# Performance work log

Measured on AMD Instinct MI355X. Metric: run time of the kernel, lower is better.

Reference implementation:

```python
import jax, jax.numpy as jnp
import numpy as np

B, S, I, H = 128, 512, 256, 512


def _lstm_last_hidden(x, W_ih, W_hh, b_ih, b_hh):
    """Single-layer unidirectional LSTM (PyTorch gate order i,f,g,o).
    x: [B,S,I]; returns final hidden state h_n [B,H]."""
    Hd = W_hh.shape[1]
    # Precompute input-side gate activations for all timesteps: [S,B,4H]
    xg = jnp.einsum('bsi,gi->sbg', x, W_ih) + b_ih + b_hh

    def step(carry, gx):
        h, c = carry
        g = gx + h @ W_hh.T  # [B,4H]
        i, f, gg, o = jnp.split(g, 4, axis=-1)
        i = jax.nn.sigmoid(i)
        f = jax.nn.sigmoid(f)
        gg = jnp.tanh(gg)
        o = jax.nn.sigmoid(o)
        c = f * c + i * gg
        h = o * jnp.tanh(c)
        return (h, c), None

    h0 = jnp.zeros((x.shape[0], Hd), x.dtype)
    (h_n, _), _ = jax.lax.scan(step, (h0, h0), xg)
    return h_n


def setup_inputs() -> dict:
    key = jax.random.key(0)
    k1, k2, k3, k4, k5, k6 = jax.random.split(key, 6)
    s = 1.0 / np.sqrt(H)  # PyTorch LSTM init scale
    return {
        'text_one': jax.random.normal(k1, (B, S, I), jnp.float32),
        'text_two': jax.random.normal(k2, (B, S, I), jnp.float32),
        'W_ih': jax.random.normal(k3, (4 * H, I), jnp.float32) * s,
        'W_hh': jax.random.normal(k4, (4 * H, H), jnp.float32) * s,
        'b_ih': jax.random.normal(k5, (4 * H,), jnp.float32) * s,
        'b_hh': jax.random.normal(k6, (4 * H,), jnp.float32) * s,
    }


def reference(text_one, text_two, W_ih, W_hh, b_ih, b_hh):
    out1 = _lstm_last_hidden(text_one, W_ih, W_hh, b_ih, b_hh)
    out2 = _lstm_last_hidden(text_two, W_ih, W_hh, b_ih, b_hh)
    return (out1, out2)
```

## Files before the change

### kernel.cpp

```cpp
#include <hip/hip_runtime.h>
#include <stdint.h>

#define SLEN    512
#define IDIM    256
#define HDIM    512
#define NROW    256
#define KP      776
#define NSTEP   512
#define NGRP    16
#define GWG     16

typedef __attribute__((ext_vector_type(8))) _Float16 half8;
typedef __attribute__((ext_vector_type(4))) float   f32x4;
typedef __attribute__((ext_vector_type(4))) int     i32x4;

#define AS1 __attribute__((address_space(1)))
#define AS3 __attribute__((address_space(3)))

__device__ __forceinline__ float sigm(float x)   { return 1.0f / (1.0f + __expf(-x)); }
__device__ __forceinline__ float tanh_f(float x) { return 2.0f / (1.0f + __expf(-2.0f * x)) - 1.0f; }

__device__ __forceinline__ half8 cvt8(float4 a, float4 b) {
    half8 v;
    v[0] = (_Float16)a.x; v[1] = (_Float16)a.y; v[2] = (_Float16)a.z; v[3] = (_Float16)a.w;
    v[4] = (_Float16)b.x; v[5] = (_Float16)b.y; v[6] = (_Float16)b.z; v[7] = (_Float16)b.w;
    return v;
}
__device__ __forceinline__ half8 cvt8i(i32x4 a, i32x4 b) {
    float4 fa = *(float4*)&a, fb = *(float4*)&b;
    return cvt8(fa, fb);
}

union hu { _Float16 h; unsigned short u; };

__global__ __launch_bounds__(256, 1)
void lstm_persistent(const float* __restrict__ x0, const float* __restrict__ x1,
                     const float* __restrict__ wih, const float* __restrict__ whh,
                     const float* __restrict__ bih, const float* __restrict__ bhh,
                     _Float16* __restrict__ hb, int* __restrict__ flg,
                     float* __restrict__ out) {
    __shared__ __align__(16) _Float16 Ab[16 * KP];

    const int tid  = threadIdx.x;
    const int lane = tid & 63;
    const int w    = tid >> 6;
    const int quad = lane >> 4;
    const int l16  = lane & 15;
    const int igrp = blockIdx.x & 15;
    const int jcg  = blockIdx.x >> 4;

    const int q0  = l16 & 3, ccl = l16 >> 2;
    const int colb = jcg * 32 + w * 8 + ccl * 2;
    const int gc0 = q0 * HDIM + colb;
    const int gc1 = gc0 + 1;
    half8 wf0[24], wf1[24];
#pragma unroll
    for (int kk = 0; kk < 24; ++kk) {
        int k0 = kk * 32 + quad * 8;
        const float* sA = (k0 < IDIM) ? wih + (size_t)gc0 * IDIM + k0
                                      : whh + (size_t)gc0 * HDIM + (k0 - IDIM);
        const float* sB = (k0 < IDIM) ? wih + (size_t)gc1 * IDIM + k0
                                      : whh + (size_t)gc1 * HDIM + (k0 - IDIM);
        wf0[kk] = cvt8(*(const float4*)sA, *(const float4*)(sA + 4));
        wf1[kk] = cvt8(*(const float4*)sB, *(const float4*)(sB + 4));
    }

    float bias0[4], bias1[4];
#pragma unroll
    for (int q = 0; q < 4; ++q) {
        int g0 = q * HDIM + jcg * 32 + w * 8 + quad * 2;
        bias0[q] = bih[g0] + bhh[g0];
        bias1[q] = bih[g0 + 1] + bhh[g0 + 1];
    }

    const float* xp  = (igrp < 8) ? x0 : x1;
    const int   brow = (igrp & 7) * 16;
    const int   r0   = tid >> 5;
    const int   o0   = (tid & 31) * 8;
    const int   grow = igrp * 16 + l16;
    const int   cc0  = jcg * 32 + w * 8 + quad * 2;

    const int* fpoll = flg + igrp * 64 + lane;
    int*       fmine = flg + igrp * 64 + jcg * 4 + w;

    float c0 = 0.f, c1 = 0.f;
    int gaveup = 0;

    {
        const float* xr0 = xp + ((size_t)(brow + r0) * SLEN + 0) * IDIM + o0;
        const float* xr1 = xr0 + (size_t)8 * SLEN * IDIM;
        float4 pa = *(const float4*)xr0, pb = *(const float4*)(xr0 + 4);
        float4 pc = *(const float4*)xr1, pd = *(const float4*)(xr1 + 4);
        *(half8*)&Ab[r0 * KP + o0]       = cvt8(pa, pb);
        *(half8*)&Ab[(r0 + 8) * KP + o0] = cvt8(pc, pd);
    }
    __syncthreads();

#pragma unroll 1
    for (int t = 0; t < NSTEP; ++t) {
        if (t > 0) {
            asm volatile("s_waitcnt lgkmcnt(0)" ::: "memory");
            __builtin_amdgcn_sched_barrier(0);
            __builtin_amdgcn_s_barrier();
        }

        f32x4 acc0 = {bias0[0], bias0[1], bias0[2], bias0[3]};
        f32x4 acc1 = {bias1[0], bias1[1], bias1[2], bias1[3]};
        const _Float16* ab = &Ab[l16 * KP + quad * 8];
#pragma unroll
        for (int kk = 0; kk < 8; ++kk) {
            half8 bf = *(const half8*)(ab + kk * 32);
            acc0 = __builtin_amdgcn_mfma_f32_16x16x32_f16(wf0[kk], bf, acc0, 0, 0, 0);
            acc1 = __builtin_amdgcn_mfma_f32_16x16x32_f16(wf1[kk], bf, acc1, 0, 0, 0);
        }

        if (t > 0 && !gaveup) {
            int it = 0;
            while (true) {
                int f;
                asm volatile("global_load_dword %0, %1, off sc0 sc1\n\t"
                             "s_waitcnt vmcnt(0)"
                             : "=&v"(f) : "v"(fpoll) : "memory");
                if (__all(f >= t)) break;
                __builtin_amdgcn_s_sleep(1);
                if (++it > (1 << 20)) { gaveup = 1; break; }
            }
            __builtin_amdgcn_fence(__ATOMIC_ACQUIRE, "workgroup");
        }

        {
            const _Float16* hsrc = hb + (size_t)((t + 1) & 1) * (NROW * HDIM)
                                      + (size_t)(igrp * 16) * HDIM;
#pragma unroll
            for (int p = 0; p < 4; ++p) {
                const int r = p * 4 + w;
                const _Float16* g = hsrc + (size_t)r * HDIM + lane * 8;
                __builtin_amdgcn_global_load_lds(
                    (const AS1 void*)g, (AS3 void*)&Ab[r * KP + IDIM],
                    16, 0, 17);
            }
            asm volatile("s_waitcnt vmcnt(0)" ::: "memory");
            __builtin_amdgcn_sched_barrier(0);
        }

        i32x4 xv0, xv1, xv2, xv3;
        if (t < NSTEP - 1) {
            const float* xr0 = xp + ((size_t)(brow + r0) * SLEN + (t + 1)) * IDIM + o0;
            const float* xr1 = xr0 + (size_t)8 * SLEN * IDIM;
            asm volatile(
                "global_load_dwordx4 %0, %4, off\n\t"
                "global_load_dwordx4 %1, %4, off offset:16\n\t"
                "global_load_dwordx4 %2, %5, off\n\t"
                "global_load_dwordx4 %3, %5, off offset:16"
                : "=&v"(xv0), "=&v"(xv1), "=&v"(xv2), "=&v"(xv3)
                : "v"(xr0), "v"(xr1)
                : "memory");
        }
        __builtin_amdgcn_sched_barrier(0);
        __builtin_amdgcn_s_barrier();

#pragma unroll
        for (int kk = 8; kk < 24; ++kk) {
            half8 bf = *(const half8*)(ab + kk * 32);
            acc0 = __builtin_amdgcn_mfma_f32_16x16x32_f16(wf0[kk], bf, acc0, 0, 0, 0);
            acc1 = __builtin_amdgcn_mfma_f32_16x16x32_f16(wf1[kk], bf, acc1, 0, 0, 0);
        }

        float i0 = sigm(acc0[0]), f0 = sigm(acc0[1]), g0 = tanh_f(acc0[2]), o0g = sigm(acc0[3]);
        c0 = f0 * c0 + i0 * g0;
        float h0 = o0g * tanh_f(c0);
        float i1 = sigm(acc1[0]), f1 = sigm(acc1[1]), g1 = tanh_f(acc1[2]), o1g = sigm(acc1[3]);
        c1 = f1 * c1 + i1 * g1;
        float h1 = o1g * tanh_f(c1);

        if (t < NSTEP - 1) {
            _Float16* hd = hb + (size_t)(t & 1) * (NROW * HDIM) + (size_t)grow * HDIM;
            hu u0; u0.h = (_Float16)h0;
            hu u1; u1.h = (_Float16)h1;
            unsigned int hp = (unsigned int)u0.u | ((unsigned int)u1.u << 16);
            asm volatile("global_store_dword %0, %1, off sc0 sc1"
                         :: "v"((int*)(hd + cc0)), "v"(hp) : "memory");
            __builtin_amdgcn_sched_barrier(0);
            asm volatile("s_waitcnt vmcnt(0)" ::: "memory");
            __builtin_amdgcn_sched_barrier(0);
            if (lane == 0) {
                int fv = t + 1;
                asm volatile("global_store_dword %0, %1, off sc0 sc1"
                             :: "v"(fmine), "v"(fv) : "memory");
            }
            *(half8*)&Ab[r0 * KP + o0]       = cvt8i(xv0, xv1);
            *(half8*)&Ab[(r0 + 8) * KP + o0] = cvt8i(xv2, xv3);
        } else {
            float2 ov; ov.x = h0; ov.y = h1;
            *(float2*)(out + (size_t)grow * HDIM + cc0) = ov;
        }
    }
}

extern "C" void kernel_launch(void* const* d_in, const int* in_sizes, int n_in,
                              void* d_out, int out_size, void* d_ws, size_t ws_size,
                              hipStream_t stream) {
    const float* x0  = (const float*)d_in[0];
    const float* x1  = (const float*)d_in[1];
    const float* wih = (const float*)d_in[2];
    const float* whh = (const float*)d_in[3];
    const float* bih = (const float*)d_in[4];
    const float* bhh = (const float*)d_in[5];

    _Float16* hb = (_Float16*)d_ws;
    int* flg = (int*)((char*)d_ws + (size_t)2 * NROW * HDIM * sizeof(_Float16));
    size_t zbytes = (size_t)2 * NROW * HDIM * sizeof(_Float16)
                  + (size_t)NGRP * 64 * sizeof(int);
    hipMemsetAsync(d_ws, 0, zbytes, stream);

    lstm_persistent<<<dim3(256), dim3(256), 0, stream>>>(
        x0, x1, wih, whh, bih, bhh, hb, flg, (float*)d_out);
}
```

Measured before the change: 1.563 ms.

## Keep x operand in registers and prefetch flag poll to skip LDS barrier

Each lane now loads its own slice of the next timestep's input directly into registers and feeds it to the MFMA B operand, so x no longer passes through LDS. This removes the top-of-loop lgkmcnt wait and workgroup barrier. It also issues a speculative flag load right after publishing h, so the spin loop can be skipped when the neighbours have already finished. The cost is 16 redundant, less coalesced global loads per lane per step (each 16-lane column group re-reads x), plus extra VGPR pressure on top of the 48 weight fragments.

```diff
diff --git a/kernel.cpp b/kernel.cpp
--- a/kernel.cpp
+++ b/kernel.cpp
@@ -5,7 +5,7 @@
 #define IDIM    256
 #define HDIM    512
 #define NROW    256
-#define KP      776
+#define HPH     520
 #define NSTEP   512
 #define NGRP    16
 #define GWG     16
@@ -26,10 +26,6 @@
     v[4] = (_Float16)b.x; v[5] = (_Float16)b.y; v[6] = (_Float16)b.z; v[7] = (_Float16)b.w;
     return v;
 }
-__device__ __forceinline__ half8 cvt8i(i32x4 a, i32x4 b) {
-    float4 fa = *(float4*)&a, fb = *(float4*)&b;
-    return cvt8(fa, fb);
-}
 
 union hu { _Float16 h; unsigned short u; };
 
@@ -39,7 +35,7 @@
                      const float* __restrict__ bih, const float* __restrict__ bhh,
                      _Float16* __restrict__ hb, int* __restrict__ flg,
                      float* __restrict__ out) {
-    __shared__ __align__(16) _Float16 Ab[16 * KP];
+    __shared__ __align__(16) _Float16 Abh[16 * HPH];
 
     const int tid  = threadIdx.x;
     const int lane = tid & 63;
@@ -75,55 +71,50 @@
 
     const float* xp  = (igrp < 8) ? x0 : x1;
     const int   brow = (igrp & 7) * 16;
-    const int   r0   = tid >> 5;
-    const int   o0   = (tid & 31) * 8;
     const int   grow = igrp * 16 + l16;
     const int   cc0  = jcg * 32 + w * 8 + quad * 2;
 
+    const float* xrow = xp + (size_t)(brow + l16) * SLEN * IDIM + quad * 8;
+
     const int* fpoll = flg + igrp * 64 + lane;
     int*       fmine = flg + igrp * 64 + jcg * 4 + w;
 
     float c0 = 0.f, c1 = 0.f;
     int gaveup = 0;
-
-    {
-        const float* xr0 = xp + ((size_t)(brow + r0) * SLEN + 0) * IDIM + o0;
-        const float* xr1 = xr0 + (size_t)8 * SLEN * IDIM;
-        float4 pa = *(const float4*)xr0, pb = *(const float4*)(xr0 + 4);
-        float4 pc = *(const float4*)xr1, pd = *(const float4*)(xr1 + 4);
-        *(half8*)&Ab[r0 * KP + o0]       = cvt8(pa, pb);
-        *(half8*)&Ab[(r0 + 8) * KP + o0] = cvt8(pc, pd);
-    }
-    __syncthreads();
+    int pf = 0;
+
+    half8 xf[8];
+#pragma unroll
+    for (int kk = 0; kk < 8; ++kk) {
+        const float* p = xrow + (size_t)kk * 32;
+        xf[kk] = cvt8(*(const float4*)p, *(const float4*)(p + 4));
+    }
 
 #pragma unroll 1
     for (int t = 0; t < NSTEP; ++t) {
-        if (t > 0) {
-            asm volatile("s_waitcnt lgkmcnt(0)" ::: "memory");
-            __builtin_amdgcn_sched_barrier(0);
-            __builtin_amdgcn_s_barrier();
-        }
-
         f32x4 acc0 = {bias0[0], bias0[1], bias0[2], bias0[3]};
         f32x4 acc1 = {bias1[0], bias1[1], bias1[2], bias1[3]};
-        const _Float16* ab = &Ab[l16 * KP + quad * 8];
 #pragma unroll
         for (int kk = 0; kk < 8; ++kk) {
-            half8 bf = *(const half8*)(ab + kk * 32);
-            acc0 = __builtin_amdgcn_mfma_f32_16x16x32_f16(wf0[kk], bf, acc0, 0, 0, 0);
-            acc1 = __builtin_amdgcn_mfma_f32_16x16x32_f16(wf1[kk], bf, acc1, 0, 0, 0);
-        }
+            acc0 = __builtin_amdgcn_mfma_f32_16x16x32_f16(wf0[kk], xf[kk], acc0, 0, 0, 0);
+            acc1 = __builtin_amdgcn_mfma_f32_16x16x32_f16(wf1[kk], xf[kk], acc1, 0, 0, 0);
+        }
+        __builtin_amdgcn_sched_barrier(0);
 
         if (t > 0 && !gaveup) {
-            int it = 0;
-            while (true) {
-                int f;
-                asm volatile("global_load_dword %0, %1, off sc0 sc1\n\t"
-                             "s_waitcnt vmcnt(0)"
-                             : "=&v"(f) : "v"(fpoll) : "memory");
-                if (__all(f >= t)) break;
-                __builtin_amdgcn_s_sleep(1);
-                if (++it > (1 << 20)) { gaveup = 1; break; }
+            asm volatile("s_waitcnt vmcnt(0)" ::: "memory");
+            __builtin_amdgcn_sched_barrier(0);
+            if (!__all(pf >= t)) {
+                int it = 0;
+                while (true) {
+                    int f;
+                    asm volatile("global_load_dword %0, %1, off sc0 sc1\n\t"
+                                 "s_waitcnt vmcnt(0)"
+                                 : "=&v"(f) : "v"(fpoll) : "memory");
+                    if (__all(f >= t)) break;
+                    __builtin_amdgcn_s_sleep(1);
+                    if (++it > (1 << 20)) { gaveup = 1; break; }
+                }
             }
             __builtin_amdgcn_fence(__ATOMIC_ACQUIRE, "workgroup");
         }
@@ -136,34 +127,51 @@
                 const int r = p * 4 + w;
                 const _Float16* g = hsrc + (size_t)r * HDIM + lane * 8;
                 __builtin_amdgcn_global_load_lds(
-                    (const AS1 void*)g, (AS3 void*)&Ab[r * KP + IDIM],
+                    (const AS1 void*)g, (AS3 void*)&Abh[r * HPH],
                     16, 0, 17);
             }
             asm volatile("s_waitcnt vmcnt(0)" ::: "memory");
             __builtin_amdgcn_sched_barrier(0);
         }
 
-        i32x4 xv0, xv1, xv2, xv3;
+        i32x4 xr0_, xr1_, xr2_, xr3_, xr4_, xr5_, xr6_, xr7_;
+        i32x4 xr8_, xr9_, xrA_, xrB_, xrC_, xrD_, xrE_, xrF_;
         if (t < NSTEP - 1) {
-            const float* xr0 = xp + ((size_t)(brow + r0) * SLEN + (t + 1)) * IDIM + o0;
-            const float* xr1 = xr0 + (size_t)8 * SLEN * IDIM;
+            const float* xb = xrow + (size_t)(t + 1) * IDIM;
             asm volatile(
-                "global_load_dwordx4 %0, %4, off\n\t"
-                "global_load_dwordx4 %1, %4, off offset:16\n\t"
-                "global_load_dwordx4 %2, %5, off\n\t"
-                "global_load_dwordx4 %3, %5, off offset:16"
-                : "=&v"(xv0), "=&v"(xv1), "=&v"(xv2), "=&v"(xv3)
-                : "v"(xr0), "v"(xr1)
-                : "memory");
+                "global_load_dwordx4 %0, %8, off\n\t"
+                "global_load_dwordx4 %1, %8, off offset:16\n\t"
+                "global_load_dwordx4 %2, %8, off offset:128\n\t"
+                "global_load_dwordx4 %3, %8, off offset:144\n\t"
+                "global_load_dwordx4 %4, %8, off offset:256\n\t"
+                "global_load_dwordx4 %5, %8, off offset:272\n\t"
+                "global_load_dwordx4 %6, %8, off offset:384\n\t"
+                "global_load_dwordx4 %7, %8, off offset:400"
+                : "=&v"(xr0_), "=&v"(xr1_), "=&v"(xr2_), "=&v"(xr3_),
+                  "=&v"(xr4_), "=&v"(xr5_), "=&v"(xr6_), "=&v"(xr7_)
+                : "v"(xb) : "memory");
+            asm volatile(
+                "global_load_dwordx4 %0, %8, off offset:512\n\t"
+                "global_load_dwordx4 %1, %8, off offset:528\n\t"
+                "global_load_dwordx4 %2, %8, off offset:640\n\t"
+                "global_load_dwordx4 %3, %8, off offset:656\n\t"
+                "global_load_dwordx4 %4, %8, off offset:768\n\t"
+                "global_load_dwordx4 %5, %8, off offset:784\n\t"
+                "global_load_dwordx4 %6, %8, off offset:896\n\t"
+                "global_load_dwordx4 %7, %8, off offset:912"
+                : "=&v"(xr8_), "=&v"(xr9_), "=&v"(xrA_), "=&v"(xrB_),
+                  "=&v"(xrC_), "=&v"(xrD_), "=&v"(xrE_), "=&v"(xrF_)
+                : "v"(xb) : "memory");
         }
         __builtin_amdgcn_sched_barrier(0);
         __builtin_amdgcn_s_barrier();
 
-#pragma unroll
-        for (int kk = 8; kk < 24; ++kk) {
-            half8 bf = *(const half8*)(ab + kk * 32);
-            acc0 = __builtin_amdgcn_mfma_f32_16x16x32_f16(wf0[kk], bf, acc0, 0, 0, 0);
-            acc1 = __builtin_amdgcn_mfma_f32_16x16x32_f16(wf1[kk], bf, acc1, 0, 0, 0);
+        const _Float16* abh = &Abh[l16 * HPH + quad * 8];
+#pragma unroll
+        for (int kk = 0; kk < 16; ++kk) {
+            half8 bf = *(const half8*)(abh + kk * 32);
+            acc0 = __builtin_amdgcn_mfma_f32_16x16x32_f16(wf0[8 + kk], bf, acc0, 0, 0, 0);
+            acc1 = __builtin_amdgcn_mfma_f32_16x16x32_f16(wf1[8 + kk], bf, acc1, 0, 0, 0);
         }
 
         float i0 = sigm(acc0[0]), f0 = sigm(acc0[1]), g0 = tanh_f(acc0[2]), o0g = sigm(acc0[3]);
@@ -188,8 +196,17 @@
                 asm volatile("global_store_dword %0, %1, off sc0 sc1"
                              :: "v"(fmine), "v"(fv) : "memory");
             }
-            *(half8*)&Ab[r0 * KP + o0]       = cvt8i(xv0, xv1);
-            *(half8*)&Ab[(r0 + 8) * KP + o0] = cvt8i(xv2, xv3);
+            asm volatile("v_mov_b32 %0, 0\n\t"
+                         "global_load_dword %0, %1, off sc0 sc1"
+                         : "=&v"(pf) : "v"(fpoll) : "memory");
+            xf[0] = cvt8(*(float4*)&xr0_, *(float4*)&xr1_);
+            xf[1] = cvt8(*(float4*)&xr2_, *(float4*)&xr3_);
+            xf[2] = cvt8(*(float4*)&xr4_, *(float4*)&xr5_);
+            xf[3] = cvt8(*(float4*)&xr6_, *(float4*)&xr7_);
+            xf[4] = cvt8(*(float4*)&xr8_, *(float4*)&xr9_);
+            xf[5] = cvt8(*(float4*)&xrA_, *(float4*)&xrB_);
+            xf[6] = cvt8(*(float4*)&xrC_, *(float4*)&xrD_);
+            xf[7] = cvt8(*(float4*)&xrE_, *(float4*)&xrF_);
         } else {
             float2 ov; ov.x = h0; ov.y = h1;
             *(float2*)(out + (size_t)grow * HDIM + cc0) = ov;
```

After: 4.275 ms. 174% more time.

## Double-buffer h and x in LDS, keep x fragments in registers, split MFMA chains

Applied to the files above, without the earlier changes.

Splits the shared LDS tile into double-buffered h (fp16) and x (fp32) buffers. Next-step x is now loaded directly into LDS with global_load_lds instead of through registers, and the x operand is converted once into register fragments. The flag poll load is issued before the input-side MFMAs so its latency overlaps them, and the top-of-loop barrier is removed. The recurrent MFMA chain is split into two accumulators to cut dependency stalls. In exchange it uses more LDS and registers, and dropping the barrier relies on double buffering for correctness.

```diff
diff --git a/kernel.cpp b/kernel.cpp
--- a/kernel.cpp
+++ b/kernel.cpp
@@ -5,14 +5,14 @@
 #define IDIM    256
 #define HDIM    512
 #define NROW    256
-#define KP      776
+#define HPH     520
+#define XPF     260
 #define NSTEP   512
 #define NGRP    16
 #define GWG     16
 
 typedef __attribute__((ext_vector_type(8))) _Float16 half8;
 typedef __attribute__((ext_vector_type(4))) float   f32x4;
-typedef __attribute__((ext_vector_type(4))) int     i32x4;
 
 #define AS1 __attribute__((address_space(1)))
 #define AS3 __attribute__((address_space(3)))
@@ -26,10 +26,6 @@
     v[4] = (_Float16)b.x; v[5] = (_Float16)b.y; v[6] = (_Float16)b.z; v[7] = (_Float16)b.w;
     return v;
 }
-__device__ __forceinline__ half8 cvt8i(i32x4 a, i32x4 b) {
-    float4 fa = *(float4*)&a, fb = *(float4*)&b;
-    return cvt8(fa, fb);
-}
 
 union hu { _Float16 h; unsigned short u; };
 
@@ -39,7 +35,8 @@
                      const float* __restrict__ bih, const float* __restrict__ bhh,
                      _Float16* __restrict__ hb, int* __restrict__ flg,
                      float* __restrict__ out) {
-    __shared__ __align__(16) _Float16 Ab[16 * KP];
+    __shared__ __align__(16) _Float16 Hb[2][16 * HPH];
+    __shared__ __align__(16) float    Xb[2][16 * XPF];
 
     const int tid  = threadIdx.x;
     const int lane = tid & 63;
@@ -75,8 +72,6 @@
 
     const float* xp  = (igrp < 8) ? x0 : x1;
     const int   brow = (igrp & 7) * 16;
-    const int   r0   = tid >> 5;
-    const int   o0   = (tid & 31) * 8;
     const int   grow = igrp * 16 + l16;
     const int   cc0  = jcg * 32 + w * 8 + quad * 2;
 
@@ -86,44 +81,57 @@
     float c0 = 0.f, c1 = 0.f;
     int gaveup = 0;
 
+    half8 xf[8];
     {
-        const float* xr0 = xp + ((size_t)(brow + r0) * SLEN + 0) * IDIM + o0;
-        const float* xr1 = xr0 + (size_t)8 * SLEN * IDIM;
-        float4 pa = *(const float4*)xr0, pb = *(const float4*)(xr0 + 4);
-        float4 pc = *(const float4*)xr1, pd = *(const float4*)(xr1 + 4);
-        *(half8*)&Ab[r0 * KP + o0]       = cvt8(pa, pb);
-        *(half8*)&Ab[(r0 + 8) * KP + o0] = cvt8(pc, pd);
-    }
-    __syncthreads();
+#pragma unroll
+        for (int p = 0; p < 4; ++p) {
+            const int r = p * 4 + w;
+            const float* g = xp + (size_t)(brow + r) * SLEN * IDIM + lane * 4;
+            __builtin_amdgcn_global_load_lds(
+                (const AS1 void*)g, (AS3 void*)&Xb[0][r * XPF], 16, 0, 0);
+        }
+        asm volatile("s_waitcnt vmcnt(0)" ::: "memory");
+        __builtin_amdgcn_sched_barrier(0);
+        __builtin_amdgcn_s_barrier();
+        const float* xb = &Xb[0][l16 * XPF + quad * 8];
+#pragma unroll
+        for (int kk = 0; kk < 8; ++kk)
+            xf[kk] = cvt8(*(const float4*)(xb + kk * 32),
+                          *(const float4*)(xb + kk * 32 + 4));
+    }
 
 #pragma unroll 1
     for (int t = 0; t < NSTEP; ++t) {
+        int f0 = 0;
         if (t > 0) {
-            asm volatile("s_waitcnt lgkmcnt(0)" ::: "memory");
-            __builtin_amdgcn_sched_barrier(0);
-            __builtin_amdgcn_s_barrier();
+            asm volatile("global_load_dword %0, %1, off sc0 sc1"
+                         : "=&v"(f0) : "v"(fpoll) : "memory");
+            __builtin_amdgcn_sched_barrier(0);
         }
 
         f32x4 acc0 = {bias0[0], bias0[1], bias0[2], bias0[3]};
         f32x4 acc1 = {bias1[0], bias1[1], bias1[2], bias1[3]};
-        const _Float16* ab = &Ab[l16 * KP + quad * 8];
 #pragma unroll
         for (int kk = 0; kk < 8; ++kk) {
-            half8 bf = *(const half8*)(ab + kk * 32);
-            acc0 = __builtin_amdgcn_mfma_f32_16x16x32_f16(wf0[kk], bf, acc0, 0, 0, 0);
-            acc1 = __builtin_amdgcn_mfma_f32_16x16x32_f16(wf1[kk], bf, acc1, 0, 0, 0);
-        }
+            acc0 = __builtin_amdgcn_mfma_f32_16x16x32_f16(wf0[kk], xf[kk], acc0, 0, 0, 0);
+            acc1 = __builtin_amdgcn_mfma_f32_16x16x32_f16(wf1[kk], xf[kk], acc1, 0, 0, 0);
+        }
+        __builtin_amdgcn_sched_barrier(0);
 
         if (t > 0 && !gaveup) {
-            int it = 0;
-            while (true) {
-                int f;
-                asm volatile("global_load_dword %0, %1, off sc0 sc1\n\t"
-                             "s_waitcnt vmcnt(0)"
-                             : "=&v"(f) : "v"(fpoll) : "memory");
-                if (__all(f >= t)) break;
-                __builtin_amdgcn_s_sleep(1);
-                if (++it > (1 << 20)) { gaveup = 1; break; }
+            asm volatile("s_waitcnt vmcnt(0)" ::: "memory");
+            __builtin_amdgcn_sched_barrier(0);
+            if (!__all(f0 >= t)) {
+                int it = 0;
+                while (true) {
+                    int f;
+                    asm volatile("global_load_dword %0, %1, off sc0 sc1\n\t"
+                                 "s_waitcnt vmcnt(0)"
+                                 : "=&v"(f) : "v"(fpoll) : "memory");
+                    if (__all(f >= t)) break;
+                    __builtin_amdgcn_s_sleep(1);
+                    if (++it > (1 << 20)) { gaveup = 1; break; }
+                }
             }
             __builtin_amdgcn_fence(__ATOMIC_ACQUIRE, "workgroup");
         }
@@ -134,43 +142,47 @@
 #pragma unroll
             for (int p = 0; p < 4; ++p) {
                 const int r = p * 4 + w;
-                const _Float16* g = hsrc + (size_t)r * HDIM + lane * 8;
                 __builtin_amdgcn_global_load_lds(
-                    (const AS1 void*)g, (AS3 void*)&Ab[r * KP + IDIM],
-                    16, 0, 17);
-            }
-            asm volatile("s_waitcnt vmcnt(0)" ::: "memory");
-            __builtin_amdgcn_sched_barrier(0);
-        }
-
-        i32x4 xv0, xv1, xv2, xv3;
-        if (t < NSTEP - 1) {
-            const float* xr0 = xp + ((size_t)(brow + r0) * SLEN + (t + 1)) * IDIM + o0;
-            const float* xr1 = xr0 + (size_t)8 * SLEN * IDIM;
-            asm volatile(
-                "global_load_dwordx4 %0, %4, off\n\t"
-                "global_load_dwordx4 %1, %4, off offset:16\n\t"
-                "global_load_dwordx4 %2, %5, off\n\t"
-                "global_load_dwordx4 %3, %5, off offset:16"
-                : "=&v"(xv0), "=&v"(xv1), "=&v"(xv2), "=&v"(xv3)
-                : "v"(xr0), "v"(xr1)
-                : "memory");
-        }
+                    (const AS1 void*)(hsrc + (size_t)r * HDIM + lane * 8),
+                    (AS3 void*)&Hb[t & 1][r * HPH], 16, 0, 17);
+            }
+            if (t < NSTEP - 1) {
+#pragma unroll
+                for (int p = 0; p < 4; ++p) {
+                    const int r = p * 4 + w;
+                    const float* g = xp + (size_t)(brow + r) * SLEN * IDIM
+                                        + (size_t)(t + 1) * IDIM + lane * 4;
+                    __builtin_amdgcn_global_load_lds(
+                        (const AS1 void*)g, (AS3 void*)&Xb[(t + 1) & 1][r * XPF],
+                        16, 0, 0);
+                }
+            }
+        }
+        asm volatile("s_waitcnt vmcnt(0)" ::: "memory");
         __builtin_amdgcn_sched_barrier(0);
         __builtin_amdgcn_s_barrier();
 
-#pragma unroll
-        for (int kk = 8; kk < 24; ++kk) {
-            half8 bf = *(const half8*)(ab + kk * 32);
-            acc0 = __builtin_amdgcn_mfma_f32_16x16x32_f16(wf0[kk], bf, acc0, 0, 0, 0);
-            acc1 = __builtin_amdgcn_mfma_f32_16x16x32_f16(wf1[kk], bf, acc1, 0, 0, 0);
-        }
-
-        float i0 = sigm(acc0[0]), f0 = sigm(acc0[1]), g0 = tanh_f(acc0[2]), o0g = sigm(acc0[3]);
-        c0 = f0 * c0 + i0 * g0;
+        {
+            const _Float16* abh = &Hb[t & 1][l16 * HPH + quad * 8];
+            f32x4 b0 = {0.f, 0.f, 0.f, 0.f}, b1 = {0.f, 0.f, 0.f, 0.f};
+#pragma unroll
+            for (int kk = 0; kk < 16; kk += 2) {
+                half8 bfa = *(const half8*)(abh + kk * 32);
+                half8 bfb = *(const half8*)(abh + (kk + 1) * 32);
+                acc0 = __builtin_amdgcn_mfma_f32_16x16x32_f16(wf0[8 + kk], bfa, acc0, 0, 0, 0);
+                b0   = __builtin_amdgcn_mfma_f32_16x16x32_f16(wf0[9 + kk], bfb, b0, 0, 0, 0);
+                acc1 = __builtin_amdgcn_mfma_f32_16x16x32_f16(wf1[8 + kk], bfa, acc1, 0, 0, 0);
+                b1   = __builtin_amdgcn_mfma_f32_16x16x32_f16(wf1[9 + kk], bfb, b1, 0, 0, 0);
+            }
+            acc0 += b0;
+            acc1 += b1;
+        }
+
+        float i0 = sigm(acc0[0]), f0g = sigm(acc0[1]), g0 = tanh_f(acc0[2]), o0g = sigm(acc0[3]);
+        c0 = f0g * c0 + i0 * g0;
         float h0 = o0g * tanh_f(c0);
-        float i1 = sigm(acc1[0]), f1 = sigm(acc1[1]), g1 = tanh_f(acc1[2]), o1g = sigm(acc1[3]);
-        c1 = f1 * c1 + i1 * g1;
+        float i1 = sigm(acc1[0]), f1g = sigm(acc1[1]), g1 = tanh_f(acc1[2]), o1g = sigm(acc1[3]);
+        c1 = f1g * c1 + i1 * g1;
         float h1 = o1g * tanh_f(c1);
 
         if (t < NSTEP - 1) {
@@ -188,8 +200,11 @@
                 asm volatile("global_store_dword %0, %1, off sc0 sc1"
                              :: "v"(fmine), "v"(fv) : "memory");
             }
-            *(half8*)&Ab[r0 * KP + o0]       = cvt8i(xv0, xv1);
-            *(half8*)&Ab[(r0 + 8) * KP + o0] = cvt8i(xv2, xv3);
+            const float* xb = &Xb[(t + 1) & 1][l16 * XPF + quad * 8];
+#pragma unroll
+            for (int kk = 0; kk < 8; ++kk)
+                xf[kk] = cvt8(*(const float4*)(xb + kk * 32),
+                              *(const float4*)(xb + kk * 32 + 4));
         } else {
             float2 ov; ov.x = h0; ov.y = h1;
             *(float2*)(out + (size_t)grow * HDIM + cc0) = ov;
```

Result: slower. 1.749 ms (+11.9%).
